# Kernel optimization log

Measured on AMD Instinct MI355X. Metric: run time of the kernel, lower is better.

Reference implementation:

```python
import jax, jax.numpy as jnp
import numpy as np
import math

# module hyperparameters (init_kwargs)
C_H = 128
K = 8
INP_SIZE = 256
S_MIN = 1.0
S_MAX_OOD = 30.0
SIGMA = 0.8
BQ = 131072


def setup_inputs() -> dict:
    key = jax.random.key(0)
    k1, k2, k3 = jax.random.split(key, 3)
    h = jax.random.normal(k1, (BQ, C_H, K), dtype=jnp.float32)
    cell = jax.random.uniform(k2, (BQ, 2), dtype=jnp.float32)
    # kaiming_uniform with a=sqrt(5) on a [3, C_h] weight -> bound = 1/sqrt(C_h)
    bound = 1.0 / math.sqrt(C_H)
    to_rgb_weight = jax.random.uniform(k3, (K, 3, C_H), dtype=jnp.float32,
                                       minval=-bound, maxval=bound)
    to_rgb_bias = jnp.zeros((K, 3), dtype=jnp.float32)
    return {"h": h, "cell": cell, "to_rgb_weight": to_rgb_weight,
            "to_rgb_bias": to_rgb_bias}


def reference(h, cell, to_rgb_weight, to_rgb_bias):
    # tau: [BQ]
    cell_geomean = jnp.maximum(jnp.sqrt(cell[:, 0] * cell[:, 1]), 1e-10)
    log_s = math.log(2.0 / INP_SIZE) - jnp.log(cell_geomean)
    tau = (K - 1) * (log_s - math.log(S_MIN)) / (math.log(S_MAX_OOD) - math.log(S_MIN))
    tau = jnp.clip(tau, 0.0, K - 1)

    # alpha: [BQ, K] Gaussian softmax over scales
    k_idx = jnp.arange(K, dtype=jnp.float32)[None, :]            # [1, K]
    logits = -(k_idx - tau[:, None]) ** 2 / (2.0 * SIGMA ** 2)   # [BQ, K]
    alpha = jax.nn.softmax(logits, axis=1)

    # per-k projection C_h -> 3: h is [BQ, C_h, K]
    rgb_k = jnp.einsum('bck,koc->bko', h, to_rgb_weight) + to_rgb_bias[None]  # [BQ, K, 3]
    y_eq = jnp.sum(alpha[:, :, None] * rgb_k, axis=1)            # [BQ, 3]
    return y_eq
```

## Files before the change

kernel.cpp:

```cpp
#include <hip/hip_runtime.h>
#include <math.h>


#define C_H   128
#define KSC   8

constexpr int NBLOCKS  = 2048;
constexpr int NTHREADS = 256;
constexpr int NWAVES   = NBLOCKS * NTHREADS / 64;

__global__ __launch_bounds__(NTHREADS)
void gsr_kernel(const float* __restrict__ h,
                const float* __restrict__ cell,
                const float* __restrict__ w,
                const float* __restrict__ bias,
                float* __restrict__ out,
                int bq)
{
    const int lane   = threadIdx.x & 63;
    const int waveId = blockIdx.x * (NTHREADS / 64) + (threadIdx.x >> 6);

    const int kbase = (lane & 1) * 4;
    const int chalf = lane >> 1;
    float wreg[4][4][3];
    #pragma unroll
    for (int i4 = 0; i4 < 4; ++i4) {
        #pragma unroll
        for (int e = 0; e < 4; ++e) {
            const int k = kbase + e;
            const int c = i4 * 32 + chalf;
            #pragma unroll
            for (int o = 0; o < 3; ++o)
                wreg[i4][e][o] = w[k * (3*C_H) + o * C_H + c];
        }
    }
    float breg[4][3];
    #pragma unroll
    for (int e = 0; e < 4; ++e)
        #pragma unroll
        for (int o = 0; o < 3; ++o)
            breg[e][o] = (lane < 2) ? bias[(kbase + e) * 3 + o] : 0.0f;

    const float inv_two_sigma_sq = 0.78125f;
    const float log_2_over_inp   = -4.8520302639196171f;
    const float seven_over_log30 = 2.0580814087539097f;

    const int ngrp = bq >> 2;
    const float2* cell2 = (const float2*)cell;

    for (int grp = waveId; grp < ngrp; grp += NWAVES) {
        const int b4 = grp << 2;

        const float4* hp = (const float4*)(h + (size_t)b4 * (C_H * KSC));
        float4 hv[16];
        #pragma unroll
        for (int i = 0; i < 16; ++i)
            hv[i] = hp[i * 64 + lane];

        float al[4][4];
        float acc[4][3];
        #pragma unroll
        for (int g = 0; g < 4; ++g) {
            const float2 cg = cell2[b4 + g];
            const float geo = fmaxf(sqrtf(cg.x * cg.y), 1e-10f);
            const float log_s = log_2_over_inp - __logf(geo);
            float tau = seven_over_log30 * log_s;
            tau = fminf(fmaxf(tau, 0.0f), 7.0f);

            float ek[8], s = 0.0f;
            #pragma unroll
            for (int k = 0; k < 8; ++k) {
                const float d = (float)k - tau;
                ek[k] = __expf(-d * d * inv_two_sigma_sq);
                s += ek[k];
            }
            const float inv = 1.0f / s;
            #pragma unroll
            for (int e = 0; e < 4; ++e)
                al[g][e] = ((lane & 1) ? ek[4 + e] : ek[e]) * inv;

            #pragma unroll
            for (int o = 0; o < 3; ++o) {
                acc[g][o] = al[g][0] * breg[0][o];
                #pragma unroll
                for (int e = 1; e < 4; ++e)
                    acc[g][o] = fmaf(al[g][e], breg[e][o], acc[g][o]);
            }
        }

        #pragma unroll
        for (int i = 0; i < 16; ++i) {
            const int g  = i >> 2;
            const int i4 = i & 3;
            const float he[4] = {hv[i].x, hv[i].y, hv[i].z, hv[i].w};
            #pragma unroll
            for (int e = 0; e < 4; ++e) {
                const float ha = he[e] * al[g][e];
                #pragma unroll
                for (int o = 0; o < 3; ++o)
                    acc[g][o] = fmaf(ha, wreg[i4][e][o], acc[g][o]);
            }
        }

        #pragma unroll
        for (int off = 32; off > 0; off >>= 1) {
            #pragma unroll
            for (int g = 0; g < 4; ++g) {
                acc[g][0] += __shfl_xor(acc[g][0], off, 64);
                acc[g][1] += __shfl_xor(acc[g][1], off, 64);
                acc[g][2] += __shfl_xor(acc[g][2], off, 64);
            }
        }

        if (lane == 0) {
            float4* op = (float4*)(out + (size_t)b4 * 3);
            op[0] = make_float4(acc[0][0], acc[0][1], acc[0][2], acc[1][0]);
            op[1] = make_float4(acc[1][1], acc[1][2], acc[2][0], acc[2][1]);
            op[2] = make_float4(acc[2][2], acc[3][0], acc[3][1], acc[3][2]);
        }
    }
}

extern "C" void kernel_launch(void* const* d_in, const int* in_sizes, int n_in,
                              void* d_out, int out_size, void* d_ws, size_t ws_size,
                              hipStream_t stream) {
    const float* h    = (const float*)d_in[0];
    const float* cell = (const float*)d_in[1];
    const float* w    = (const float*)d_in[2];
    const float* bias = (const float*)d_in[3];
    float* out = (float*)d_out;
    const int bq = in_sizes[0] / (C_H * KSC);

    gsr_kernel<<<NBLOCKS, NTHREADS, 0, stream>>>(h, cell, w, bias, out, bq);
}
```

Before: 682.0 us.

## Software-pipeline h loads with double buffering and shrink per-wave group to two rows

Restructures the grid-stride loop so each wave prefetches the next group's h and cell data into a second register buffer while it computes the current group. The group size drops from four rows to two to keep the doubled register footprint manageable, and launch bounds now request 3 blocks per SM. The aim is to hide global memory latency in this bandwidth-bound kernel. The costs are more loop iterations, smaller output stores, and register pressure that could limit occupancy.

New measurement: 1.094 ms. +60.4%, slower.

```diff
diff --git a/kernel.cpp b/kernel.cpp
--- a/kernel.cpp
+++ b/kernel.cpp
@@ -9,7 +9,7 @@
 constexpr int NTHREADS = 256;
 constexpr int NWAVES   = NBLOCKS * NTHREADS / 64;
 
-__global__ __launch_bounds__(NTHREADS)
+__global__ __launch_bounds__(NTHREADS, 3)
 void gsr_kernel(const float* __restrict__ h,
                 const float* __restrict__ cell,
                 const float* __restrict__ w,
@@ -19,6 +19,9 @@
 {
     const int lane   = threadIdx.x & 63;
     const int waveId = blockIdx.x * (NTHREADS / 64) + (threadIdx.x >> 6);
+
+    const int ngrp = bq >> 1;
+    if (waveId >= ngrp) return;
 
     const int kbase = (lane & 1) * 4;
     const int chalf = lane >> 1;
@@ -45,27 +48,26 @@
     const float log_2_over_inp   = -4.8520302639196171f;
     const float seven_over_log30 = 2.0580814087539097f;
 
-    const int ngrp = bq >> 2;
-    const float2* cell2 = (const float2*)cell;
+    const float4* cell4 = (const float4*)cell;
 
-    for (int grp = waveId; grp < ngrp; grp += NWAVES) {
-        const int b4 = grp << 2;
+    auto issue = [&](int g, float4& cv, float4 (&hv)[8]) {
+        cv = cell4[g];
+        const float4* hp = (const float4*)(h + (size_t)g * (2 * C_H * KSC));
+        #pragma unroll
+        for (int i = 0; i < 8; ++i)
+            hv[i] = hp[i * 64 + lane];
+    };
 
-        const float4* hp = (const float4*)(h + (size_t)b4 * (C_H * KSC));
-        float4 hv[16];
+    auto compute = [&](int g, const float4& cv, const float4 (&hv)[8]) {
+        float al[2][4];
+        float acc[2][3];
         #pragma unroll
-        for (int i = 0; i < 16; ++i)
-            hv[i] = hp[i * 64 + lane];
-
-        float al[4][4];
-        float acc[4][3];
-        #pragma unroll
-        for (int g = 0; g < 4; ++g) {
-            const float2 cg = cell2[b4 + g];
-            const float geo = fmaxf(sqrtf(cg.x * cg.y), 1e-10f);
+        for (int q = 0; q < 2; ++q) {
+            const float cx = q ? cv.z : cv.x;
+            const float cy = q ? cv.w : cv.y;
+            const float geo   = fmaxf(sqrtf(cx * cy), 1e-10f);
             const float log_s = log_2_over_inp - __logf(geo);
-            float tau = seven_over_log30 * log_s;
-            tau = fminf(fmaxf(tau, 0.0f), 7.0f);
+            float tau = fminf(fmaxf(seven_over_log30 * log_s, 0.0f), 7.0f);
 
             float ek[8], s = 0.0f;
             #pragma unroll
@@ -77,46 +79,72 @@
             const float inv = 1.0f / s;
             #pragma unroll
             for (int e = 0; e < 4; ++e)
-                al[g][e] = ((lane & 1) ? ek[4 + e] : ek[e]) * inv;
+                al[q][e] = ((lane & 1) ? ek[4 + e] : ek[e]) * inv;
 
             #pragma unroll
             for (int o = 0; o < 3; ++o) {
-                acc[g][o] = al[g][0] * breg[0][o];
+                acc[q][o] = al[q][0] * breg[0][o];
                 #pragma unroll
                 for (int e = 1; e < 4; ++e)
-                    acc[g][o] = fmaf(al[g][e], breg[e][o], acc[g][o]);
+                    acc[q][o] = fmaf(al[q][e], breg[e][o], acc[q][o]);
             }
         }
 
         #pragma unroll
-        for (int i = 0; i < 16; ++i) {
-            const int g  = i >> 2;
+        for (int i = 0; i < 8; ++i) {
+            const int q  = i >> 2;
             const int i4 = i & 3;
             const float he[4] = {hv[i].x, hv[i].y, hv[i].z, hv[i].w};
             #pragma unroll
             for (int e = 0; e < 4; ++e) {
-                const float ha = he[e] * al[g][e];
+                const float ha = he[e] * al[q][e];
                 #pragma unroll
                 for (int o = 0; o < 3; ++o)
-                    acc[g][o] = fmaf(ha, wreg[i4][e][o], acc[g][o]);
+                    acc[q][o] = fmaf(ha, wreg[i4][e][o], acc[q][o]);
             }
         }
 
         #pragma unroll
         for (int off = 32; off > 0; off >>= 1) {
             #pragma unroll
-            for (int g = 0; g < 4; ++g) {
-                acc[g][0] += __shfl_xor(acc[g][0], off, 64);
-                acc[g][1] += __shfl_xor(acc[g][1], off, 64);
-                acc[g][2] += __shfl_xor(acc[g][2], off, 64);
+            for (int q = 0; q < 2; ++q) {
+                acc[q][0] += __shfl_xor(acc[q][0], off, 64);
+                acc[q][1] += __shfl_xor(acc[q][1], off, 64);
+                acc[q][2] += __shfl_xor(acc[q][2], off, 64);
             }
         }
 
         if (lane == 0) {
-            float4* op = (float4*)(out + (size_t)b4 * 3);
-            op[0] = make_float4(acc[0][0], acc[0][1], acc[0][2], acc[1][0]);
-            op[1] = make_float4(acc[1][1], acc[1][2], acc[2][0], acc[2][1]);
-            op[2] = make_float4(acc[2][2], acc[3][0], acc[3][1], acc[3][2]);
+            float2* op = (float2*)(out + (size_t)g * 6);
+            op[0] = make_float2(acc[0][0], acc[0][1]);
+            op[1] = make_float2(acc[0][2], acc[1][0]);
+            op[2] = make_float2(acc[1][1], acc[1][2]);
+        }
+    };
+
+    float4 cva, cvb;
+    float4 hva[8], hvb[8];
+
+    int g = waveId;
+    issue(g, cva, hva);
+    for (;;) {
+        int gn = g + NWAVES;
+        if (gn < ngrp) {
+            issue(gn, cvb, hvb);
+            compute(g, cva, hva);
+            g = gn;
+        } else {
+            compute(g, cva, hva);
+            break;
+        }
+        gn = g + NWAVES;
+        if (gn < ngrp) {
+            issue(gn, cva, hva);
+            compute(g, cvb, hvb);
+            g = gn;
+        } else {
+            compute(g, cvb, hvb);
+            break;
         }
     }
 }
```

## Double-buffer h loads across wave iterations with two-row groups

Applied to the files above, without the earlier changes.

Each wave now processes two rows per iteration instead of four and software-pipelines its global loads: it issues the next group's h and cell loads into a second register set before computing the current group, with a sched_barrier to keep the loads early. Launch bounds now request two blocks per SM and the output writes are narrowed to float2. The aim is to hide HBM latency in this streaming kernel by keeping loads in flight during the FMA and shuffle-reduction phase. The cost is doubled register buffers and twice as many per-group shuffle reductions relative to the data moved, and the launch-bounds change may lead to register spills.

Measured after the change: 855.0 us. +25.4%, slower.

```diff
diff --git a/kernel.cpp b/kernel.cpp
--- a/kernel.cpp
+++ b/kernel.cpp
@@ -9,7 +9,69 @@
 constexpr int NTHREADS = 256;
 constexpr int NWAVES   = NBLOCKS * NTHREADS / 64;
 
-__global__ __launch_bounds__(NTHREADS)
+#define ISSUE(S, g_) do {                                                     \
+    cv##S = cell4[g_];                                                        \
+    const float4* hp_ = (const float4*)(h + (size_t)(g_) * (2 * C_H * KSC));  \
+    h##S##0 = hp_[0*64 + lane];  h##S##1 = hp_[1*64 + lane];                  \
+    h##S##2 = hp_[2*64 + lane];  h##S##3 = hp_[3*64 + lane];                  \
+    h##S##4 = hp_[4*64 + lane];  h##S##5 = hp_[5*64 + lane];                  \
+    h##S##6 = hp_[6*64 + lane];  h##S##7 = hp_[7*64 + lane];                  \
+    __builtin_amdgcn_sched_barrier(0);                                        \
+} while (0)
+
+#define ACC4(hv_, q_, i4_) do {                                               \
+    const float he_[4] = {hv_.x, hv_.y, hv_.z, hv_.w};                        \
+    _Pragma("unroll") for (int e = 0; e < 4; ++e) {                           \
+        const float ha_ = he_[e] * al[q_][e];                                 \
+        _Pragma("unroll") for (int o = 0; o < 3; ++o)                         \
+            acc[q_][o] = fmaf(ha_, wreg[i4_][e][o], acc[q_][o]);              \
+    }                                                                         \
+} while (0)
+
+#define COMPUTE(S, g_) do {                                                   \
+    float al[2][4];                                                           \
+    float acc[2][3];                                                          \
+    _Pragma("unroll") for (int q = 0; q < 2; ++q) {                           \
+        const float cx_ = q ? cv##S.z : cv##S.x;                              \
+        const float cy_ = q ? cv##S.w : cv##S.y;                              \
+        const float geo_   = fmaxf(sqrtf(cx_ * cy_), 1e-10f);                 \
+        const float log_s_ = log_2_over_inp - __logf(geo_);                   \
+        float tau_ = fminf(fmaxf(seven_over_log30 * log_s_, 0.0f), 7.0f);     \
+        float ek_[8], s_ = 0.0f;                                              \
+        _Pragma("unroll") for (int k = 0; k < 8; ++k) {                       \
+            const float d_ = (float)k - tau_;                                 \
+            ek_[k] = __expf(-d_ * d_ * inv_two_sigma_sq);                     \
+            s_ += ek_[k];                                                     \
+        }                                                                     \
+        const float inv_ = 1.0f / s_;                                         \
+        _Pragma("unroll") for (int e = 0; e < 4; ++e)                         \
+            al[q][e] = ((lane & 1) ? ek_[4 + e] : ek_[e]) * inv_;             \
+        _Pragma("unroll") for (int o = 0; o < 3; ++o) {                       \
+            acc[q][o] = al[q][0] * breg[0][o];                                \
+            _Pragma("unroll") for (int e = 1; e < 4; ++e)                     \
+                acc[q][o] = fmaf(al[q][e], breg[e][o], acc[q][o]);            \
+        }                                                                     \
+    }                                                                         \
+    ACC4(h##S##0, 0, 0);  ACC4(h##S##1, 0, 1);                                \
+    ACC4(h##S##2, 0, 2);  ACC4(h##S##3, 0, 3);                                \
+    ACC4(h##S##4, 1, 0);  ACC4(h##S##5, 1, 1);                                \
+    ACC4(h##S##6, 1, 2);  ACC4(h##S##7, 1, 3);                                \
+    _Pragma("unroll") for (int off = 32; off > 0; off >>= 1) {                \
+        _Pragma("unroll") for (int q = 0; q < 2; ++q) {                       \
+            acc[q][0] += __shfl_xor(acc[q][0], off, 64);                      \
+            acc[q][1] += __shfl_xor(acc[q][1], off, 64);                      \
+            acc[q][2] += __shfl_xor(acc[q][2], off, 64);                      \
+        }                                                                     \
+    }                                                                         \
+    if (lane == 0) {                                                          \
+        float2* op_ = (float2*)(out + (size_t)(g_) * 6);                      \
+        op_[0] = make_float2(acc[0][0], acc[0][1]);                           \
+        op_[1] = make_float2(acc[0][2], acc[1][0]);                           \
+        op_[2] = make_float2(acc[1][1], acc[1][2]);                           \
+    }                                                                         \
+} while (0)
+
+__global__ __launch_bounds__(NTHREADS, 2)
 void gsr_kernel(const float* __restrict__ h,
                 const float* __restrict__ cell,
                 const float* __restrict__ w,
@@ -19,6 +81,9 @@
 {
     const int lane   = threadIdx.x & 63;
     const int waveId = blockIdx.x * (NTHREADS / 64) + (threadIdx.x >> 6);
+
+    const int ngrp = bq >> 1;
+    if (waveId >= ngrp) return;
 
     const int kbase = (lane & 1) * 4;
     const int chalf = lane >> 1;
@@ -45,79 +110,24 @@
     const float log_2_over_inp   = -4.8520302639196171f;
     const float seven_over_log30 = 2.0580814087539097f;
 
-    const int ngrp = bq >> 2;
-    const float2* cell2 = (const float2*)cell;
+    const float4* cell4 = (const float4*)cell;
 
-    for (int grp = waveId; grp < ngrp; grp += NWAVES) {
-        const int b4 = grp << 2;
+    float4 cvA, cvB;
+    float4 hA0, hA1, hA2, hA3, hA4, hA5, hA6, hA7;
+    float4 hB0, hB1, hB2, hB3, hB4, hB5, hB6, hB7;
 
-        const float4* hp = (const float4*)(h + (size_t)b4 * (C_H * KSC));
-        float4 hv[16];
-        #pragma unroll
-        for (int i = 0; i < 16; ++i)
-            hv[i] = hp[i * 64 + lane];
-
-        float al[4][4];
-        float acc[4][3];
-        #pragma unroll
-        for (int g = 0; g < 4; ++g) {
-            const float2 cg = cell2[b4 + g];
-            const float geo = fmaxf(sqrtf(cg.x * cg.y), 1e-10f);
-            const float log_s = log_2_over_inp - __logf(geo);
-            float tau = seven_over_log30 * log_s;
-            tau = fminf(fmaxf(tau, 0.0f), 7.0f);
-
-            float ek[8], s = 0.0f;
-            #pragma unroll
-            for (int k = 0; k < 8; ++k) {
-                const float d = (float)k - tau;
-                ek[k] = __expf(-d * d * inv_two_sigma_sq);
-                s += ek[k];
-            }
-            const float inv = 1.0f / s;
-            #pragma unroll
-            for (int e = 0; e < 4; ++e)
-                al[g][e] = ((lane & 1) ? ek[4 + e] : ek[e]) * inv;
-
-            #pragma unroll
-            for (int o = 0; o < 3; ++o) {
-                acc[g][o] = al[g][0] * breg[0][o];
-                #pragma unroll
-                for (int e = 1; e < 4; ++e)
-                    acc[g][o] = fmaf(al[g][e], breg[e][o], acc[g][o]);
-            }
-        }
-
-        #pragma unroll
-        for (int i = 0; i < 16; ++i) {
-            const int g  = i >> 2;
-            const int i4 = i & 3;
-            const float he[4] = {hv[i].x, hv[i].y, hv[i].z, hv[i].w};
-            #pragma unroll
-            for (int e = 0; e < 4; ++e) {
-                const float ha = he[e] * al[g][e];
-                #pragma unroll
-                for (int o = 0; o < 3; ++o)
-                    acc[g][o] = fmaf(ha, wreg[i4][e][o], acc[g][o]);
-            }
-        }
-
-        #pragma unroll
-        for (int off = 32; off > 0; off >>= 1) {
-            #pragma unroll
-            for (int g = 0; g < 4; ++g) {
-                acc[g][0] += __shfl_xor(acc[g][0], off, 64);
-                acc[g][1] += __shfl_xor(acc[g][1], off, 64);
-                acc[g][2] += __shfl_xor(acc[g][2], off, 64);
-            }
-        }
-
-        if (lane == 0) {
-            float4* op = (float4*)(out + (size_t)b4 * 3);
-            op[0] = make_float4(acc[0][0], acc[0][1], acc[0][2], acc[1][0]);
-            op[1] = make_float4(acc[1][1], acc[1][2], acc[2][0], acc[2][1]);
-            op[2] = make_float4(acc[2][2], acc[3][0], acc[3][1], acc[3][2]);
-        }
+    int g  = waveId;
+    ISSUE(A, g);
+    int gn = g + NWAVES;
+    while (true) {
+        if (gn >= ngrp) { COMPUTE(A, g); break; }
+        ISSUE(B, gn);
+        COMPUTE(A, g);
+        g = gn;  gn += NWAVES;
+        if (gn >= ngrp) { COMPUTE(B, g); break; }
+        ISSUE(A, gn);
+        COMPUTE(B, g);
+        g = gn;  gn += NWAVES;
     }
 }
 
```
